# Performance work log

Measured on AMD Instinct MI355X. Metric: run time of the kernel, lower is better.

## Reference

```python
import jax, jax.numpy as jnp
import numpy as np
from jax import lax

B, H, W = 8, 500, 500
M = 2048          # per-image cap on active bottleneck voxels (ragged -> fixed)
GRID = 125        # bottleneck grid size
ENC_RANGE = 125.0
HEADS, ATTN_CH, CH = 4, 128, 64
EPS = 1e-5
NEG = -1e9

def _conv(x, w, b, stride, pad):
    y = lax.conv_general_dilated(x, w, (stride, stride), pad,
                                 dimension_numbers=('NCHW', 'HWIO', 'NCHW'))
    return y + b[None, :, None, None]

def _maxpool2(m):
    return lax.reduce_window(m, -jnp.inf, lax.max, (1, 1, 2, 2), (1, 1, 2, 2), 'VALID')

def setup_inputs():
    key = jax.random.key(0)
    ks = jax.random.split(key, 12)
    occ = (jax.random.uniform(ks[0], (B, 1, H, W)) < 0.005).astype(jnp.float32)
    x = jax.random.normal(ks[1], (B, 1, H, W), dtype=jnp.float32) * occ
    def rn(k, shape, scale):
        return jax.random.normal(k, shape, dtype=jnp.float32) * scale
    return {
        'x': x,
        'w0': rn(ks[2], (3, 3, 1, 32), 0.3), 'b0': jnp.zeros(32, jnp.float32),
        'g0': jnp.ones(32, jnp.float32), 'be0': jnp.zeros(32, jnp.float32),
        'w1': rn(ks[3], (2, 2, 32, 64), 0.1), 'b1': jnp.zeros(64, jnp.float32),
        'g1': jnp.ones(64, jnp.float32), 'be1': jnp.zeros(64, jnp.float32),
        'w2': rn(ks[4], (2, 2, 64, 64), 0.08), 'b2': jnp.zeros(64, jnp.float32),
        'g2': jnp.ones(64, jnp.float32), 'be2': jnp.zeros(64, jnp.float32),
        'wpe': rn(ks[5], (2, 2, CH), 0.5), 'bpe': jnp.zeros((2, CH), jnp.float32),
        'wq': rn(ks[6], (2, CH, ATTN_CH), 0.12), 'bq': jnp.zeros((2, ATTN_CH), jnp.float32),
        'wk': rn(ks[7], (2, CH, ATTN_CH), 0.12), 'bk': jnp.zeros((2, ATTN_CH), jnp.float32),
        'wv': rn(ks[8], (2, CH, ATTN_CH), 0.12), 'bv': jnp.zeros((2, ATTN_CH), jnp.float32),
        'wo': rn(ks[9], (2, ATTN_CH, CH), 0.09), 'bo': jnp.zeros((2, CH), jnp.float32),
        'wh': rn(ks[10], (CH, 4), 0.12), 'bh': jnp.zeros(4, jnp.float32),
    }

def reference(x, w0, b0, g0, be0, w1, b1, g1, be1, w2, b2, g2, be2,
              wpe, bpe, wq, bq, wk, bk, wv, bv, wo, bo, wh, bh):
    # active-site mask (Voxels.from_dense)
    mask0 = (x != 0).any(axis=1, keepdims=True).astype(x.dtype)   # [B,1,500,500]

    def bn_relu(y, g, be):
        # eval-mode BatchNorm1d over active voxel features (running stats 0/1)
        return jax.nn.relu(g[None, :, None, None] * y / jnp.sqrt(1.0 + EPS)
                           + be[None, :, None, None])

    # enc0: submanifold 3x3/s1 -> active set unchanged; inactive inputs are zero
    y = bn_relu(_conv(x, w0, b0, 1, 'SAME'), g0, be0) * mask0
    # enc1/enc2: strided 2x2/s2 -> output active iff any input in window active
    mask1 = _maxpool2(mask0)
    y = bn_relu(_conv(y, w1, b1, 2, 'VALID'), g1, be1) * mask1
    mask2 = _maxpool2(mask1)
    y = bn_relu(_conv(y, w2, b2, 2, 'VALID'), g2, be2) * mask2    # [B,64,125,125]

    # gather active bottleneck voxels per image (ragged -> fixed M + validity mask)
    mflat = mask2.reshape(B, GRID * GRID)
    vals, idx = lax.top_k(mflat, M)     # active-first; stable tie-break (lowest idx)
    valid = vals                        # [B,M] in {0,1}
    feats = jnp.take_along_axis(
        y.reshape(B, CH, GRID * GRID).transpose(0, 2, 1),
        idx[:, :, None], axis=1)        # [B,M,64]
    pos = jnp.stack([idx // GRID, idx % GRID], axis=-1).astype(x.dtype) / ENC_RANGE

    dh = ATTN_CH // HEADS
    kmask = (1.0 - valid)[:, None, None, :] * NEG
    for i in range(2):  # N_ATTN structurally distinct layers
        pe = pos @ wpe[i] + bpe[i]
        h = feats + pe
        q = (h @ wq[i] + bq[i]).reshape(B, M, HEADS, dh)
        k = (h @ wk[i] + bk[i]).reshape(B, M, HEADS, dh)
        v = (h @ wv[i] + bv[i]).reshape(B, M, HEADS, dh)
        s = jnp.einsum('bqhd,bkhd->bhqk', q, k) / jnp.sqrt(jnp.asarray(dh, x.dtype))
        a = jax.nn.softmax(s + kmask, axis=-1)
        o = jnp.einsum('bhqk,bkhd->bqhd', a, v).reshape(B, M, ATTN_CH)
        feats = (feats + o @ wo[i] + bo[i]) * valid[..., None]

    # sparse_global_avg_pool: mean over active voxels per image
    counts = jnp.clip(valid.sum(axis=1, keepdims=True), 1.0, None)
    pooled = feats.sum(axis=1) / counts                            # [B,64]
    return pooled @ wh + bh                                        # [B,4]
```

## Files before the change

kernel.cpp:

```cpp
#include <hip/hip_runtime.h>

#define BDIM   8
#define NPIX   250000
#define G1N    62500
#define G2N    15625
#define NB0    977
#define NB1    245
#define NB2    62
#define CAP0   4096
#define CAP1   4096
#define CAPM   2048
#define CH     64
#define ACH    128
#define NHEADS 4
#define DH     32

static constexpr float BN_INV    = 0.99999500003749969f;
static constexpr float ATT_SCALE = 0.17677669529663687f;

typedef _Float16 f16x8 __attribute__((ext_vector_type(8)));
typedef float f32x4 __attribute__((ext_vector_type(4)));

static constexpr size_t E_MAP0  = 0;
static constexpr size_t E_MAP1  = E_MAP0 + (size_t)BDIM*NPIX;
static constexpr size_t E_CNT   = E_MAP1 + (size_t)BDIM*G1N;
static constexpr size_t E_ZEND  = E_CNT + 32;
static constexpr size_t E_BC    = E_ZEND;
static constexpr size_t E_BO    = E_BC + (size_t)3*BDIM*1024;
static constexpr size_t E_BM    = E_BO + (size_t)3*BDIM*1024;
static constexpr size_t E_LIST0 = E_BM + (size_t)3*BDIM*1024*8;
static constexpr size_t E_LIST1 = E_LIST0 + (size_t)BDIM*CAP0;
static constexpr size_t E_LIST2 = E_LIST1 + (size_t)BDIM*CAP1;
static constexpr size_t E_Y0    = E_LIST2 + (size_t)BDIM*CAPM;
static constexpr size_t E_Y1    = E_Y0 + (size_t)BDIM*CAP0*32;
static constexpr size_t E_FE    = E_Y1 + (size_t)BDIM*CAP1*64;
static constexpr size_t E_QF    = E_FE + (size_t)BDIM*CAPM*64;
static constexpr size_t E_KF    = E_QF + (size_t)32*CAPM*32/2;
static constexpr size_t E_VT    = E_KF + (size_t)32*CAPM*32/2;
static constexpr size_t E_PART  = E_VT + (size_t)32*CAPM*32/2;


__device__ __forceinline__ bool act0(const float* x, int pix, int b) {
  return (pix < NPIX) && (x[(size_t)b * NPIX + pix] != 0.f);
}
__device__ __forceinline__ bool act1(const int* map0, int p, int b) {
  if (p >= G1N) return false;
  int i = p / 250, j = p - i * 250;
  const int* m = map0 + (size_t)b * NPIX + (2 * i) * 500 + 2 * j;
  return (m[0] | m[1] | m[500] | m[501]) != 0;
}
__device__ __forceinline__ bool act2(const int* map1, int p, int b) {
  if (p >= G2N) return false;
  int i = p / 125, j = p - i * 125;
  const int* m = map1 + (size_t)b * G1N + (2 * i) * 250 + 2 * j;
  return (m[0] | m[1] | m[250] | m[251]) != 0;
}

#define COUNT_BODY(ACT_EXPR)                                            \
  int idx = blockIdx.x * 256 + threadIdx.x;                             \
  int b = blockIdx.y;                                                   \
  bool act = (ACT_EXPR);                                                \
  unsigned long long mask = __ballot(act);                              \
  __shared__ int wc[4];                                                 \
  if ((threadIdx.x & 63) == 0) {                                        \
    wc[threadIdx.x >> 6] = __popcll(mask);                              \
    bm[((size_t)b * 1024 + blockIdx.x) * 4 + (threadIdx.x >> 6)] = mask;\
  }                                                                     \
  __syncthreads();                                                      \
  if (threadIdx.x == 0)                                                 \
    bcnt[b * 1024 + blockIdx.x] = wc[0] + wc[1] + wc[2] + wc[3];

__global__ void k_cnt0(const float* __restrict__ x, int* __restrict__ bcnt,
                       unsigned long long* __restrict__ bm) {
  COUNT_BODY(act0(x, idx, b))
}
__global__ void k_cnt1(const int* __restrict__ map0, int* __restrict__ bcnt,
                       unsigned long long* __restrict__ bm) {
  COUNT_BODY(act1(map0, idx, b))
}
__global__ void k_cnt2(const int* __restrict__ map1, int* __restrict__ bcnt,
                       unsigned long long* __restrict__ bm) {
  COUNT_BODY(act2(map1, idx, b))
}

__global__ __launch_bounds__(256) void k_scan(const int* __restrict__ bcnt,
                                              int* __restrict__ boff,
                                              int* __restrict__ cnt,
                                              int nblk, int cbase) {
  int b = blockIdx.x;
  int t = threadIdx.x;
  int base = t * 4;
  int v[4];
  int ts = 0;
#pragma unroll
  for (int u = 0; u < 4; ++u) {
    v[u] = (base + u < nblk) ? bcnt[b * 1024 + base + u] : 0;
    ts += v[u];
  }
  int lane = t & 63, w = t >> 6;
  int incl = ts;
#pragma unroll
  for (int off = 1; off < 64; off <<= 1) {
    int o = __shfl_up(incl, off, 64);
    if (lane >= off) incl += o;
  }
  __shared__ int wsum[4];
  if (lane == 63) wsum[w] = incl;
  __syncthreads();
  int woff = 0;
#pragma unroll
  for (int k = 0; k < 3; ++k) if (k < w) woff += wsum[k];
  int run = woff + incl - ts;
#pragma unroll
  for (int u = 0; u < 4; ++u) {
    if (base + u < nblk) boff[b * 1024 + base + u] = run;
    run += v[u];
  }
  if (t == 255) cnt[cbase + b] = run;
}

#define EMIT_PROLOG                                                     \
  int idx = blockIdx.x * 256 + threadIdx.x;                             \
  int b = blockIdx.y;                                                   \
  int lane = threadIdx.x & 63;                                          \
  unsigned long long mask =                                             \
      bm[((size_t)b * 1024 + blockIdx.x) * 4 + (threadIdx.x >> 6)];     \
  bool act = (mask >> lane) & 1;                                        \
  __shared__ int wbase[4];                                              \
  if (lane == 0) wbase[threadIdx.x >> 6] = __popcll(mask);              \
  __syncthreads();                                                      \
  if (threadIdx.x == 0) {                                               \
    int s = boff[b * 1024 + blockIdx.x];                                \
    for (int w = 0; w < 4; ++w) { int c = wbase[w]; wbase[w] = s; s += c; } \
  }                                                                     \
  __syncthreads();                                                      \
  int slot = wbase[threadIdx.x >> 6] + __popcll(mask & ((1ull << lane) - 1ull));

__global__ void k_emit0(const unsigned long long* __restrict__ bm,
                        const int* __restrict__ boff,
                        int* __restrict__ map0, int* __restrict__ list0) {
  EMIT_PROLOG
  if (act && slot < CAP0) {
    list0[b * CAP0 + slot] = idx;
    map0[(size_t)b * NPIX + idx] = slot + 1;
  }
}
__global__ void k_emit1(const unsigned long long* __restrict__ bm,
                        const int* __restrict__ boff,
                        int* __restrict__ map1, int* __restrict__ list1) {
  EMIT_PROLOG
  if (act && slot < CAP1) {
    list1[b * CAP1 + slot] = idx;
    map1[(size_t)b * G1N + idx] = slot + 1;
  }
}
__global__ void k_emit2(const unsigned long long* __restrict__ bm,
                        const int* __restrict__ boff,
                        int* __restrict__ list2) {
  EMIT_PROLOG
  if (act && slot < CAPM) list2[b * CAPM + slot] = idx;
}


__global__ void k_y0(const float* __restrict__ x, const float* __restrict__ w0,
                     const float* __restrict__ b0, const float* __restrict__ g0,
                     const float* __restrict__ be0,
                     const int* __restrict__ list0, const int* __restrict__ cnt,
                     float* __restrict__ y0) {
  int t = blockIdx.x * 256 + threadIdx.x;
  int b = t >> 17;
  int r = t & 131071;
  int slot = r >> 5, c = r & 31;
  int n = min(cnt[b], CAP0);
  if (slot >= n) return;
  int pix = list0[b * CAP0 + slot];
  int i = pix / 500, j = pix - i * 500;
  float acc = b0[c];
#pragma unroll
  for (int di = 0; di < 3; ++di) {
    int ii = i + di - 1;
    if ((unsigned)ii >= 500u) continue;
#pragma unroll
    for (int dj = 0; dj < 3; ++dj) {
      int jj = j + dj - 1;
      if ((unsigned)jj >= 500u) continue;
      acc += x[(size_t)b * NPIX + ii * 500 + jj] * w0[(di * 3 + dj) * 32 + c];
    }
  }
  float o = g0[c] * acc * BN_INV + be0[c];
  y0[((size_t)(b * CAP0) + slot) * 32 + c] = fmaxf(o, 0.f);
}

__global__ void k_y1(const float* __restrict__ y0, const float* __restrict__ w1,
                     const float* __restrict__ b1, const float* __restrict__ g1,
                     const float* __restrict__ be1,
                     const int* __restrict__ map0, const int* __restrict__ list1,
                     const int* __restrict__ cnt, float* __restrict__ y1) {
  int b = blockIdx.x >> 9;
  int sblk = blockIdx.x & 511;
  int s0 = sblk * 8;
  int n = min(cnt[BDIM + b], CAP1);
  if (s0 >= n) return;
  __shared__ float inT[4][32][8];
  for (int idx = threadIdx.x; idx < 1024; idx += 64) {
    int s = idx & 7;
    int r = idx >> 3;
    int ci = r & 31, pp = r >> 5;
    float v = 0.f;
    int sg = s0 + s;
    if (sg < n) {
      int p = list1[b * CAP1 + sg];
      int i = p / 250, j = p - i * 250;
      int sm = map0[(size_t)b * NPIX + (2 * i + (pp >> 1)) * 500 + (2 * j + (pp & 1))];
      if (sm) v = y0[((size_t)(b * CAP0) + (sm - 1)) * 32 + ci];
    }
    inT[pp][ci][s] = v;
  }
  __syncthreads();
  int co = threadIdx.x;
  float acc[8];
#pragma unroll
  for (int s = 0; s < 8; ++s) acc[s] = b1[co];
#pragma unroll 2
  for (int pp = 0; pp < 4; ++pp)
    for (int ci = 0; ci < 32; ++ci) {
      float wv = w1[((pp << 5) + ci) * 64 + co];
      float4 i0 = *(const float4*)&inT[pp][ci][0];
      float4 i1 = *(const float4*)&inT[pp][ci][4];
      acc[0] += i0.x * wv; acc[1] += i0.y * wv; acc[2] += i0.z * wv; acc[3] += i0.w * wv;
      acc[4] += i1.x * wv; acc[5] += i1.y * wv; acc[6] += i1.z * wv; acc[7] += i1.w * wv;
    }
  int smax = min(8, n - s0);
  for (int s = 0; s < smax; ++s) {
    float o = g1[co] * acc[s] * BN_INV + be1[co];
    y1[((size_t)(b * CAP1) + s0 + s) * 64 + co] = fmaxf(o, 0.f);
  }
}

__global__ void k_y2(const float* __restrict__ y1, const float* __restrict__ w2,
                     const float* __restrict__ b2, const float* __restrict__ g2,
                     const float* __restrict__ be2,
                     const int* __restrict__ map1, const int* __restrict__ list2,
                     const int* __restrict__ cnt, float* __restrict__ feats) {
  int b = blockIdx.x >> 8;
  int sblk = blockIdx.x & 255;
  int s0 = sblk * 8;
  int n = min(cnt[2 * BDIM + b], CAPM);
  if (s0 >= n) return;
  __shared__ float inT[4][64][8];
  for (int idx = threadIdx.x; idx < 2048; idx += 64) {
    int s = idx & 7;
    int r = idx >> 3;
    int ci = r & 63, pp = r >> 6;
    float v = 0.f;
    int sg = s0 + s;
    if (sg < n) {
      int p = list2[b * CAPM + sg];
      int i = p / 125, j = p - i * 125;
      int sm = map1[(size_t)b * G1N + (2 * i + (pp >> 1)) * 250 + (2 * j + (pp & 1))];
      if (sm) v = y1[((size_t)(b * CAP1) + (sm - 1)) * 64 + ci];
    }
    inT[pp][ci][s] = v;
  }
  __syncthreads();
  int co = threadIdx.x;
  float acc[8];
#pragma unroll
  for (int s = 0; s < 8; ++s) acc[s] = b2[co];
#pragma unroll 2
  for (int pp = 0; pp < 4; ++pp)
    for (int ci = 0; ci < 64; ++ci) {
      float wv = w2[((pp << 6) + ci) * 64 + co];
      float4 i0 = *(const float4*)&inT[pp][ci][0];
      float4 i1 = *(const float4*)&inT[pp][ci][4];
      acc[0] += i0.x * wv; acc[1] += i0.y * wv; acc[2] += i0.z * wv; acc[3] += i0.w * wv;
      acc[4] += i1.x * wv; acc[5] += i1.y * wv; acc[6] += i1.z * wv; acc[7] += i1.w * wv;
    }
  int smax = min(8, n - s0);
  for (int s = 0; s < smax; ++s) {
    float o = g2[co] * acc[s] * BN_INV + be2[co];
    feats[((size_t)(b * CAPM) + s0 + s) * 64 + co] = fmaxf(o, 0.f);
  }
}


__global__ void k_qkv(const float* __restrict__ feats, const int* __restrict__ list2,
                      const int* __restrict__ cnt,
                      const float* __restrict__ wpe, const float* __restrict__ bpe,
                      const float* __restrict__ wq, const float* __restrict__ bq,
                      const float* __restrict__ wk, const float* __restrict__ bk,
                      const float* __restrict__ wv, const float* __restrict__ bv,
                      int layer, _Float16* __restrict__ qf, _Float16* __restrict__ kf,
                      _Float16* __restrict__ vt) {
  int b = blockIdx.x >> 7;
  int sblk = blockIdx.x & 127;
  int s0 = sblk * 16;
  int n = min(cnt[2 * BDIM + b], CAPM);
  if (s0 >= n) return;
  __shared__ float hT[64][16];
  for (int idx = threadIdx.x; idx < 1024; idx += 128) {
    int s = idx & 15, c = idx >> 4;
    float hv = 0.f;
    int sg = s0 + s;
    if (sg < n) {
      int p = list2[b * CAPM + sg];
      int i = p / 125, j = p - i * 125;
      hv = feats[((size_t)(b * CAPM) + sg) * 64 + c]
         + (float)i * (1.f / 125.f) * wpe[(layer * 2 + 0) * 64 + c]
         + (float)j * (1.f / 125.f) * wpe[(layer * 2 + 1) * 64 + c]
         + bpe[layer * 64 + c];
    }
    hT[c][s] = hv;
  }
  __syncthreads();
  int o = threadIdx.x;
  float accq[16], acck[16], accv[16];
  float bqv = bq[layer * 128 + o], bkv = bk[layer * 128 + o], bvv = bv[layer * 128 + o];
#pragma unroll
  for (int s = 0; s < 16; ++s) { accq[s] = bqv; acck[s] = bkv; accv[s] = bvv; }
  const float* wq_ = wq + (size_t)layer * 64 * 128 + o;
  const float* wk_ = wk + (size_t)layer * 64 * 128 + o;
  const float* wv_ = wv + (size_t)layer * 64 * 128 + o;
  for (int c = 0; c < 64; ++c) {
    float wqv = wq_[c * 128], wkv = wk_[c * 128], wvv = wv_[c * 128];
    float hh[16];
#pragma unroll
    for (int sq = 0; sq < 4; ++sq) {
      float4 h4 = *(const float4*)&hT[c][4 * sq];
      hh[4 * sq] = h4.x; hh[4 * sq + 1] = h4.y; hh[4 * sq + 2] = h4.z; hh[4 * sq + 3] = h4.w;
    }
#pragma unroll
    for (int s = 0; s < 16; ++s) {
      accq[s] += hh[s] * wqv; acck[s] += hh[s] * wkv; accv[s] += hh[s] * wvv;
    }
  }
  int hd = o >> 5, d = o & 31;
  size_t bh = (size_t)(b * NHEADS + hd);
  int smax = min(16, n - s0);
  for (int s = 0; s < smax; ++s) {
    size_t rb = (bh * CAPM + s0 + s) * 32 + d;
    qf[rb] = (_Float16)accq[s];
    kf[rb] = (_Float16)acck[s];
    vt[(bh * 32 + d) * CAPM + s0 + s] = (_Float16)accv[s];
  }
}


union U4H8 { uint4 u; f16x8 h; };
union PKU  { _Float16 h[2]; unsigned int u; };

__global__ __launch_bounds__(256) void k_attn(
    const _Float16* __restrict__ qf, const _Float16* __restrict__ kf,
    const _Float16* __restrict__ vt, const int* __restrict__ cnt,
    const float* __restrict__ wo, const float* __restrict__ bo, int layer,
    float* __restrict__ feats) {
  int qt = blockIdx.x & 127;
  int b  = blockIdx.x >> 7;
  int n = min(cnt[2 * BDIM + b], CAPM);
  int q0 = qt * 16;
  if (q0 >= n) return;
  int h = threadIdx.x >> 6;
  int lane = threadIdx.x & 63;
  int g = lane >> 4, qr = lane & 15;
  size_t bh = (size_t)(b * NHEADS + h) * CAPM;
  const _Float16* vbase = vt + (size_t)(b * NHEADS + h) * 32 * CAPM;
  f16x8 fq = *(const f16x8*)(qf + (bh + q0 + qr) * 32 + g * 8);
  f32x4 acc0 = {0.f, 0.f, 0.f, 0.f}, acc1 = {0.f, 0.f, 0.f, 0.f};
  float m = -1e30f, l = 0.f;
  __shared__ unsigned int P4[4][512];
  __shared__ float Lf4[4][16];
  __shared__ float Ll4[4][16];
  __shared__ float oT[128][17];
  unsigned int* P = P4[h];
  float* Lf = Lf4[h];
  int swz = (qr & 7) << 2;

  for (int t0 = 0; t0 < n; t0 += 64) {
    f32x4 st[4];
#pragma unroll
    for (int t = 0; t < 4; ++t) {
      f16x8 ka = *(const f16x8*)(kf + (bh + t0 + 16 * t + qr) * 32 + g * 8);
      f32x4 z = {0.f, 0.f, 0.f, 0.f};
      st[t] = __builtin_amdgcn_mfma_f32_16x16x32_f16(ka, fq, z, 0, 0, 0);
    }
    if (t0 + 64 > n) {
#pragma unroll
      for (int t = 0; t < 4; ++t)
#pragma unroll
        for (int r = 0; r < 4; ++r)
          if (t0 + 16 * t + 4 * g + r >= n) st[t][r] = -1e30f;
    }
    float tm = -1e30f;
#pragma unroll
    for (int t = 0; t < 4; ++t)
#pragma unroll
      for (int r = 0; r < 4; ++r) tm = fmaxf(tm, st[t][r]);
    tm = fmaxf(tm, __shfl_xor(tm, 16));
    tm = fmaxf(tm, __shfl_xor(tm, 32));
    float mn = fmaxf(m, tm * ATT_SCALE);
    float f = __expf(m - mn);
    m = mn;
    if (g == 0) Lf[qr] = f;
    float ls = 0.f;
#pragma unroll
    for (int t = 0; t < 4; ++t) {
      PKU a, c;
      float p0 = __expf(st[t][0] * ATT_SCALE - mn);
      float p1 = __expf(st[t][1] * ATT_SCALE - mn);
      float p2 = __expf(st[t][2] * ATT_SCALE - mn);
      float p3 = __expf(st[t][3] * ATT_SCALE - mn);
      a.h[0] = (_Float16)p0; a.h[1] = (_Float16)p1;
      c.h[0] = (_Float16)p2; c.h[1] = (_Float16)p3;
      ls += (float)a.h[0] + (float)a.h[1] + (float)c.h[0] + (float)c.h[1];
      int w = qr * 32 + 8 * t + 2 * g;
      P[w ^ swz] = a.u;
      P[(w + 1) ^ swz] = c.u;
    }
    ls += __shfl_xor(ls, 16);
    ls += __shfl_xor(ls, 32);
    l = l * f + ls;
    __syncthreads();
    U4H8 pa0, pa1;
    pa0.u = *(const uint4*)&P[(qr * 32 + 4 * g) ^ swz];
    pa1.u = *(const uint4*)&P[(qr * 32 + 16 + 4 * g) ^ swz];
    float fr0 = Lf[4 * g + 0], fr1 = Lf[4 * g + 1];
    float fr2 = Lf[4 * g + 2], fr3 = Lf[4 * g + 3];
    acc0[0] *= fr0; acc0[1] *= fr1; acc0[2] *= fr2; acc0[3] *= fr3;
    acc1[0] *= fr0; acc1[1] *= fr1; acc1[2] *= fr2; acc1[3] *= fr3;
    __syncthreads();
    f16x8 v00 = *(const f16x8*)(vbase + (size_t)qr * CAPM + t0 + g * 8);
    f16x8 v01 = *(const f16x8*)(vbase + (size_t)(16 + qr) * CAPM + t0 + g * 8);
    f16x8 v10 = *(const f16x8*)(vbase + (size_t)qr * CAPM + t0 + 32 + g * 8);
    f16x8 v11 = *(const f16x8*)(vbase + (size_t)(16 + qr) * CAPM + t0 + 32 + g * 8);
    acc0 = __builtin_amdgcn_mfma_f32_16x16x32_f16(pa0.h, v00, acc0, 0, 0, 0);
    acc1 = __builtin_amdgcn_mfma_f32_16x16x32_f16(pa0.h, v01, acc1, 0, 0, 0);
    acc0 = __builtin_amdgcn_mfma_f32_16x16x32_f16(pa1.h, v10, acc0, 0, 0, 0);
    acc1 = __builtin_amdgcn_mfma_f32_16x16x32_f16(pa1.h, v11, acc1, 0, 0, 0);
  }
  if (g == 0) Ll4[h][qr] = l;
  __syncthreads();
#pragma unroll
  for (int r = 0; r < 4; ++r) {
    float inv = 1.f / Ll4[h][4 * g + r];
    oT[h * 32 + qr][4 * g + r] = acc0[r] * inv;
    oT[h * 32 + 16 + qr][4 * g + r] = acc1[r] * inv;
  }
  __syncthreads();
  int co = lane;
  float pacc[4] = {0.f, 0.f, 0.f, 0.f};
  const float* w = wo + (size_t)layer * 128 * 64 + co;
  for (int c = 0; c < 128; ++c) {
    float wv = w[c * 64];
#pragma unroll
    for (int u = 0; u < 4; ++u) pacc[u] += oT[c][4 * h + u] * wv;
  }
  float bov = bo[layer * 64 + co];
#pragma unroll
  for (int u = 0; u < 4; ++u) {
    int tok = q0 + 4 * h + u;
    if (tok < n) feats[((size_t)(b * CAPM) + tok) * 64 + co] += pacc[u] + bov;
  }
}


__global__ void k_head1(const float* __restrict__ feats, const int* __restrict__ cnt,
                        float* __restrict__ part) {
  int b = blockIdx.x >> 4;
  int chunk = blockIdx.x & 15;
  int n = min(cnt[2 * BDIM + b], CAPM);
  int c = threadIdx.x & 63, sub = threadIdx.x >> 6;
  int lo = chunk * 128, hi = min(n, lo + 128);
  float s = 0.f;
  for (int mm = lo + sub; mm < hi; mm += 4)
    s += feats[((size_t)(b * CAPM) + mm) * 64 + c];
  __shared__ float red[4][64];
  red[sub][c] = s;
  __syncthreads();
  if (threadIdx.x < 64)
    part[(b * 16 + chunk) * 64 + c] = red[0][c] + red[1][c] + red[2][c] + red[3][c];
}

__global__ void k_head2(const float* __restrict__ part, const float* __restrict__ wh,
                        const float* __restrict__ bhd, const int* __restrict__ cnt,
                        float* __restrict__ out) {
  int b = blockIdx.x;
  int n = min(cnt[2 * BDIM + b], CAPM);
  int c = threadIdx.x;
  float s = 0.f;
#pragma unroll
  for (int k = 0; k < 16; ++k) s += part[(b * 16 + k) * 64 + c];
  __shared__ float pooled[64];
  pooled[c] = s / (float)max(n, 1);
  __syncthreads();
  if (c < 4) {
    float o = bhd[c];
#pragma unroll
    for (int c2 = 0; c2 < 64; ++c2) o += pooled[c2] * wh[c2 * 4 + c];
    out[b * 4 + c] = o;
  }
}


extern "C" void kernel_launch(void* const* d_in, const int* in_sizes, int n_in,
                              void* d_out, int out_size, void* d_ws, size_t ws_size,
                              hipStream_t stream) {
  const float* x   = (const float*)d_in[0];
  const float* w0  = (const float*)d_in[1];
  const float* b0  = (const float*)d_in[2];
  const float* g0  = (const float*)d_in[3];
  const float* be0 = (const float*)d_in[4];
  const float* w1  = (const float*)d_in[5];
  const float* b1  = (const float*)d_in[6];
  const float* g1  = (const float*)d_in[7];
  const float* be1 = (const float*)d_in[8];
  const float* w2  = (const float*)d_in[9];
  const float* b2  = (const float*)d_in[10];
  const float* g2  = (const float*)d_in[11];
  const float* be2 = (const float*)d_in[12];
  const float* wpe = (const float*)d_in[13];
  const float* bpe = (const float*)d_in[14];
  const float* wq  = (const float*)d_in[15];
  const float* bq  = (const float*)d_in[16];
  const float* wk  = (const float*)d_in[17];
  const float* bk  = (const float*)d_in[18];
  const float* wv  = (const float*)d_in[19];
  const float* bv  = (const float*)d_in[20];
  const float* wo  = (const float*)d_in[21];
  const float* bo  = (const float*)d_in[22];
  const float* wh  = (const float*)d_in[23];
  const float* bh  = (const float*)d_in[24];

  int* wsI = (int*)d_ws;
  float* wsF = (float*)d_ws;
  unsigned long long* bm = (unsigned long long*)(wsI + E_BM);
  _Float16* qf = (_Float16*)(wsI + E_QF);
  _Float16* kf = (_Float16*)(wsI + E_KF);
  _Float16* vt = (_Float16*)(wsI + E_VT);

  hipMemsetAsync(d_ws, 0, E_ZEND * 4, stream);

  k_cnt0<<<dim3(NB0, BDIM), 256, 0, stream>>>(x, wsI + E_BC + 0 * BDIM * 1024,
                                              bm + 0 * BDIM * 4096);
  k_scan<<<BDIM, 256, 0, stream>>>(wsI + E_BC + 0 * BDIM * 1024,
                                   wsI + E_BO + 0 * BDIM * 1024,
                                   wsI + E_CNT, NB0, 0);
  k_emit0<<<dim3(NB0, BDIM), 256, 0, stream>>>(bm + 0 * BDIM * 4096,
                                               wsI + E_BO + 0 * BDIM * 1024,
                                               wsI + E_MAP0, wsI + E_LIST0);
  k_y0<<<(BDIM * CAP0 * 32) / 256, 256, 0, stream>>>(
      x, w0, b0, g0, be0, wsI + E_LIST0, wsI + E_CNT, wsF + E_Y0);
  k_cnt1<<<dim3(NB1, BDIM), 256, 0, stream>>>(wsI + E_MAP0,
                                              wsI + E_BC + 1 * BDIM * 1024,
                                              bm + 1 * BDIM * 4096);
  k_scan<<<BDIM, 256, 0, stream>>>(wsI + E_BC + 1 * BDIM * 1024,
                                   wsI + E_BO + 1 * BDIM * 1024,
                                   wsI + E_CNT, NB1, BDIM);
  k_emit1<<<dim3(NB1, BDIM), 256, 0, stream>>>(bm + 1 * BDIM * 4096,
                                               wsI + E_BO + 1 * BDIM * 1024,
                                               wsI + E_MAP1, wsI + E_LIST1);
  k_y1<<<BDIM * (CAP1 / 8), 64, 0, stream>>>(
      wsF + E_Y0, w1, b1, g1, be1, wsI + E_MAP0, wsI + E_LIST1, wsI + E_CNT, wsF + E_Y1);
  k_cnt2<<<dim3(NB2, BDIM), 256, 0, stream>>>(wsI + E_MAP1,
                                              wsI + E_BC + 2 * BDIM * 1024,
                                              bm + 2 * BDIM * 4096);
  k_scan<<<BDIM, 256, 0, stream>>>(wsI + E_BC + 2 * BDIM * 1024,
                                   wsI + E_BO + 2 * BDIM * 1024,
                                   wsI + E_CNT, NB2, 2 * BDIM);
  k_emit2<<<dim3(NB2, BDIM), 256, 0, stream>>>(bm + 2 * BDIM * 4096,
                                               wsI + E_BO + 2 * BDIM * 1024,
                                               wsI + E_LIST2);
  k_y2<<<BDIM * (CAPM / 8), 64, 0, stream>>>(
      wsF + E_Y1, w2, b2, g2, be2, wsI + E_MAP1, wsI + E_LIST2, wsI + E_CNT, wsF + E_FE);

  for (int layer = 0; layer < 2; ++layer) {
    k_qkv<<<BDIM * (CAPM / 16), 128, 0, stream>>>(
        wsF + E_FE, wsI + E_LIST2, wsI + E_CNT, wpe, bpe, wq, bq, wk, bk, wv, bv,
        layer, qf, kf, vt);
    k_attn<<<BDIM * (CAPM / 16), 256, 0, stream>>>(
        qf, kf, vt, wsI + E_CNT, wo, bo, layer, wsF + E_FE);
  }

  k_head1<<<BDIM * 16, 256, 0, stream>>>(wsF + E_FE, wsI + E_CNT, wsF + E_PART);
  k_head2<<<BDIM, 64, 0, stream>>>(wsF + E_PART, wh, bh, wsI + E_CNT, (float*)d_out);
}
```

Baseline: 292.8 us.

## Split attention into per-head wave blocks with prefetched K/V and separate projection

Attention now runs one 64-thread block per (batch, head, query tile) with no __syncthreads, double-buffers K and V register loads one tile ahead, and passes rescale factors with shuffles instead of shared memory. The output projection moves to a new k_proj kernel that reads an intermediate fp32 buffer. Block indices interleave the batch so images with different active counts spread across CUs. This aims at more parallelism and hidden memory latency, at the cost of an extra launch and a global round-trip of the attention output.

```diff
diff --git a/kernel.cpp b/kernel.cpp
--- a/kernel.cpp
+++ b/kernel.cpp
@@ -37,7 +37,8 @@
 static constexpr size_t E_QF    = E_FE + (size_t)BDIM*CAPM*64;
 static constexpr size_t E_KF    = E_QF + (size_t)32*CAPM*32/2;
 static constexpr size_t E_VT    = E_KF + (size_t)32*CAPM*32/2;
-static constexpr size_t E_PART  = E_VT + (size_t)32*CAPM*32/2;
+static constexpr size_t E_O     = E_VT + (size_t)32*CAPM*32/2;
+static constexpr size_t E_PART  = E_O + (size_t)BDIM*CAPM*ACH;
 
 
 __device__ __forceinline__ bool act0(const float* x, int pix, int b) {
@@ -292,8 +293,8 @@
                       const float* __restrict__ wv, const float* __restrict__ bv,
                       int layer, _Float16* __restrict__ qf, _Float16* __restrict__ kf,
                       _Float16* __restrict__ vt) {
-  int b = blockIdx.x >> 7;
-  int sblk = blockIdx.x & 127;
+  int b = blockIdx.x & 7;
+  int sblk = blockIdx.x >> 3;
   int s0 = sblk * 16;
   int n = min(cnt[2 * BDIM + b], CAPM);
   if (s0 >= n) return;
@@ -349,117 +350,183 @@
 union U4H8 { uint4 u; f16x8 h; };
 union PKU  { _Float16 h[2]; unsigned int u; };
 
-__global__ __launch_bounds__(256) void k_attn(
+#define LOADK(K0, K1, K2, K3, T0)                                          \
+  K0 = *(const f16x8*)(kf + (bh + (T0) + qr) * 32 + g8);                   \
+  K1 = *(const f16x8*)(kf + (bh + (T0) + 16 + qr) * 32 + g8);              \
+  K2 = *(const f16x8*)(kf + (bh + (T0) + 32 + qr) * 32 + g8);              \
+  K3 = *(const f16x8*)(kf + (bh + (T0) + 48 + qr) * 32 + g8);
+
+#define LOADV(V0, V1, V2, V3, T0)                                          \
+  V0 = *(const f16x8*)(vbase + (size_t)qr * CAPM + (T0) + g8);             \
+  V1 = *(const f16x8*)(vbase + (size_t)(16 + qr) * CAPM + (T0) + g8);      \
+  V2 = *(const f16x8*)(vbase + (size_t)qr * CAPM + (T0) + 32 + g8);        \
+  V3 = *(const f16x8*)(vbase + (size_t)(16 + qr) * CAPM + (T0) + 32 + g8);
+
+#define PROCESS(K0, K1, K2, K3, V0, V1, V2, V3, T0)                        \
+  {                                                                        \
+    f32x4 z = {0.f, 0.f, 0.f, 0.f};                                        \
+    f32x4 st0 = __builtin_amdgcn_mfma_f32_16x16x32_f16(K0, fq, z, 0, 0, 0);\
+    f32x4 st1 = __builtin_amdgcn_mfma_f32_16x16x32_f16(K1, fq, z, 0, 0, 0);\
+    f32x4 st2 = __builtin_amdgcn_mfma_f32_16x16x32_f16(K2, fq, z, 0, 0, 0);\
+    f32x4 st3 = __builtin_amdgcn_mfma_f32_16x16x32_f16(K3, fq, z, 0, 0, 0);\
+    if ((T0) + 64 > n) {                                                   \
+      _Pragma("unroll") for (int r = 0; r < 4; ++r) {                      \
+        if ((T0) + 4 * g + r >= n)      st0[r] = -1e30f;                   \
+        if ((T0) + 16 + 4 * g + r >= n) st1[r] = -1e30f;                   \
+        if ((T0) + 32 + 4 * g + r >= n) st2[r] = -1e30f;                   \
+        if ((T0) + 48 + 4 * g + r >= n) st3[r] = -1e30f;                   \
+      }                                                                    \
+    }                                                                      \
+    float tm = st0[0];                                                     \
+    _Pragma("unroll") for (int r = 1; r < 4; ++r) tm = fmaxf(tm, st0[r]);  \
+    _Pragma("unroll") for (int r = 0; r < 4; ++r) tm = fmaxf(tm, st1[r]);  \
+    _Pragma("unroll") for (int r = 0; r < 4; ++r) tm = fmaxf(tm, st2[r]);  \
+    _Pragma("unroll") for (int r = 0; r < 4; ++r) tm = fmaxf(tm, st3[r]);  \
+    tm = fmaxf(tm, __shfl_xor(tm, 16));                                    \
+    tm = fmaxf(tm, __shfl_xor(tm, 32));                                    \
+    float mn = fmaxf(m, tm * ATT_SCALE);                                   \
+    float f_ = __expf(m - mn);                                             \
+    m = mn;                                                                \
+    float ls = 0.f;                                                        \
+    {                                                                      \
+      PKU a, c;                                                            \
+      a.h[0] = (_Float16)__expf(st0[0] * ATT_SCALE - mn);                  \
+      a.h[1] = (_Float16)__expf(st0[1] * ATT_SCALE - mn);                  \
+      c.h[0] = (_Float16)__expf(st0[2] * ATT_SCALE - mn);                  \
+      c.h[1] = (_Float16)__expf(st0[3] * ATT_SCALE - mn);                  \
+      ls += (float)a.h[0] + (float)a.h[1] + (float)c.h[0] + (float)c.h[1]; \
+      P[(qr * 32 + 0 + 2 * g) ^ swz] = a.u;                                \
+      P[(qr * 32 + 1 + 2 * g) ^ swz] = c.u;                                \
+      a.h[0] = (_Float16)__expf(st1[0] * ATT_SCALE - mn);                  \
+      a.h[1] = (_Float16)__expf(st1[1] * ATT_SCALE - mn);                  \
+      c.h[0] = (_Float16)__expf(st1[2] * ATT_SCALE - mn);                  \
+      c.h[1] = (_Float16)__expf(st1[3] * ATT_SCALE - mn);                  \
+      ls += (float)a.h[0] + (float)a.h[1] + (float)c.h[0] + (float)c.h[1]; \
+      P[(qr * 32 + 8 + 2 * g) ^ swz] = a.u;                                \
+      P[(qr * 32 + 9 + 2 * g) ^ swz] = c.u;                                \
+      a.h[0] = (_Float16)__expf(st2[0] * ATT_SCALE - mn);                  \
+      a.h[1] = (_Float16)__expf(st2[1] * ATT_SCALE - mn);                  \
+      c.h[0] = (_Float16)__expf(st2[2] * ATT_SCALE - mn);                  \
+      c.h[1] = (_Float16)__expf(st2[3] * ATT_SCALE - mn);                  \
+      ls += (float)a.h[0] + (float)a.h[1] + (float)c.h[0] + (float)c.h[1]; \
+      P[(qr * 32 + 16 + 2 * g) ^ swz] = a.u;                               \
+      P[(qr * 32 + 17 + 2 * g) ^ swz] = c.u;                               \
+      a.h[0] = (_Float16)__expf(st3[0] * ATT_SCALE - mn);                  \
+      a.h[1] = (_Float16)__expf(st3[1] * ATT_SCALE - mn);                  \
+      c.h[0] = (_Float16)__expf(st3[2] * ATT_SCALE - mn);                  \
+      c.h[1] = (_Float16)__expf(st3[3] * ATT_SCALE - mn);                  \
+      ls += (float)a.h[0] + (float)a.h[1] + (float)c.h[0] + (float)c.h[1]; \
+      P[(qr * 32 + 24 + 2 * g) ^ swz] = a.u;                               \
+      P[(qr * 32 + 25 + 2 * g) ^ swz] = c.u;                               \
+    }                                                                      \
+    ls += __shfl_xor(ls, 16);                                              \
+    ls += __shfl_xor(ls, 32);                                              \
+    l = l * f_ + ls;                                                       \
+    __builtin_amdgcn_sched_barrier(0);                                     \
+    U4H8 pa0, pa1;                                                         \
+    pa0.u = *(const uint4*)&P[(qr * 32 + 4 * g) ^ swz];                    \
+    pa1.u = *(const uint4*)&P[(qr * 32 + 16 + 4 * g) ^ swz];               \
+    float fr0 = __shfl(f_, 4 * g + 0, 16);                                 \
+    float fr1 = __shfl(f_, 4 * g + 1, 16);                                 \
+    float fr2 = __shfl(f_, 4 * g + 2, 16);                                 \
+    float fr3 = __shfl(f_, 4 * g + 3, 16);                                 \
+    acc0[0] *= fr0; acc0[1] *= fr1; acc0[2] *= fr2; acc0[3] *= fr3;        \
+    acc1[0] *= fr0; acc1[1] *= fr1; acc1[2] *= fr2; acc1[3] *= fr3;        \
+    acc0 = __builtin_amdgcn_mfma_f32_16x16x32_f16(pa0.h, V0, acc0, 0, 0, 0);\
+    acc1 = __builtin_amdgcn_mfma_f32_16x16x32_f16(pa0.h, V1, acc1, 0, 0, 0);\
+    acc0 = __builtin_amdgcn_mfma_f32_16x16x32_f16(pa1.h, V2, acc0, 0, 0, 0);\
+    acc1 = __builtin_amdgcn_mfma_f32_16x16x32_f16(pa1.h, V3, acc1, 0, 0, 0);\
+  }
+
+__global__ __launch_bounds__(64, 4) void k_attn(
     const _Float16* __restrict__ qf, const _Float16* __restrict__ kf,
     const _Float16* __restrict__ vt, const int* __restrict__ cnt,
-    const float* __restrict__ wo, const float* __restrict__ bo, int layer,
-    float* __restrict__ feats) {
-  int qt = blockIdx.x & 127;
-  int b  = blockIdx.x >> 7;
+    float* __restrict__ obuf) {
+  int b  = blockIdx.x & 7;
+  int rr = blockIdx.x >> 3;
+  int qt = rr & 127;
+  int h  = rr >> 7;
   int n = min(cnt[2 * BDIM + b], CAPM);
   int q0 = qt * 16;
   if (q0 >= n) return;
-  int h = threadIdx.x >> 6;
-  int lane = threadIdx.x & 63;
+  int lane = threadIdx.x;
   int g = lane >> 4, qr = lane & 15;
+  int g8 = g * 8;
   size_t bh = (size_t)(b * NHEADS + h) * CAPM;
   const _Float16* vbase = vt + (size_t)(b * NHEADS + h) * 32 * CAPM;
-  f16x8 fq = *(const f16x8*)(qf + (bh + q0 + qr) * 32 + g * 8);
+  f16x8 fq = *(const f16x8*)(qf + (bh + q0 + qr) * 32 + g8);
   f32x4 acc0 = {0.f, 0.f, 0.f, 0.f}, acc1 = {0.f, 0.f, 0.f, 0.f};
   float m = -1e30f, l = 0.f;
-  __shared__ unsigned int P4[4][512];
-  __shared__ float Lf4[4][16];
-  __shared__ float Ll4[4][16];
-  __shared__ float oT[128][17];
-  unsigned int* P = P4[h];
-  float* Lf = Lf4[h];
+  __shared__ unsigned int P[512];
   int swz = (qr & 7) << 2;
 
-  for (int t0 = 0; t0 < n; t0 += 64) {
-    f32x4 st[4];
-#pragma unroll
-    for (int t = 0; t < 4; ++t) {
-      f16x8 ka = *(const f16x8*)(kf + (bh + t0 + 16 * t + qr) * 32 + g * 8);
-      f32x4 z = {0.f, 0.f, 0.f, 0.f};
-      st[t] = __builtin_amdgcn_mfma_f32_16x16x32_f16(ka, fq, z, 0, 0, 0);
-    }
-    if (t0 + 64 > n) {
-#pragma unroll
-      for (int t = 0; t < 4; ++t)
-#pragma unroll
-        for (int r = 0; r < 4; ++r)
-          if (t0 + 16 * t + 4 * g + r >= n) st[t][r] = -1e30f;
-    }
-    float tm = -1e30f;
-#pragma unroll
-    for (int t = 0; t < 4; ++t)
-#pragma unroll
-      for (int r = 0; r < 4; ++r) tm = fmaxf(tm, st[t][r]);
-    tm = fmaxf(tm, __shfl_xor(tm, 16));
-    tm = fmaxf(tm, __shfl_xor(tm, 32));
-    float mn = fmaxf(m, tm * ATT_SCALE);
-    float f = __expf(m - mn);
-    m = mn;
-    if (g == 0) Lf[qr] = f;
-    float ls = 0.f;
-#pragma unroll
-    for (int t = 0; t < 4; ++t) {
-      PKU a, c;
-      float p0 = __expf(st[t][0] * ATT_SCALE - mn);
-      float p1 = __expf(st[t][1] * ATT_SCALE - mn);
-      float p2 = __expf(st[t][2] * ATT_SCALE - mn);
-      float p3 = __expf(st[t][3] * ATT_SCALE - mn);
-      a.h[0] = (_Float16)p0; a.h[1] = (_Float16)p1;
-      c.h[0] = (_Float16)p2; c.h[1] = (_Float16)p3;
-      ls += (float)a.h[0] + (float)a.h[1] + (float)c.h[0] + (float)c.h[1];
-      int w = qr * 32 + 8 * t + 2 * g;
-      P[w ^ swz] = a.u;
-      P[(w + 1) ^ swz] = c.u;
-    }
-    ls += __shfl_xor(ls, 16);
-    ls += __shfl_xor(ls, 32);
-    l = l * f + ls;
-    __syncthreads();
-    U4H8 pa0, pa1;
-    pa0.u = *(const uint4*)&P[(qr * 32 + 4 * g) ^ swz];
-    pa1.u = *(const uint4*)&P[(qr * 32 + 16 + 4 * g) ^ swz];
-    float fr0 = Lf[4 * g + 0], fr1 = Lf[4 * g + 1];
-    float fr2 = Lf[4 * g + 2], fr3 = Lf[4 * g + 3];
-    acc0[0] *= fr0; acc0[1] *= fr1; acc0[2] *= fr2; acc0[3] *= fr3;
-    acc1[0] *= fr0; acc1[1] *= fr1; acc1[2] *= fr2; acc1[3] *= fr3;
-    __syncthreads();
-    f16x8 v00 = *(const f16x8*)(vbase + (size_t)qr * CAPM + t0 + g * 8);
-    f16x8 v01 = *(const f16x8*)(vbase + (size_t)(16 + qr) * CAPM + t0 + g * 8);
-    f16x8 v10 = *(const f16x8*)(vbase + (size_t)qr * CAPM + t0 + 32 + g * 8);
-    f16x8 v11 = *(const f16x8*)(vbase + (size_t)(16 + qr) * CAPM + t0 + 32 + g * 8);
-    acc0 = __builtin_amdgcn_mfma_f32_16x16x32_f16(pa0.h, v00, acc0, 0, 0, 0);
-    acc1 = __builtin_amdgcn_mfma_f32_16x16x32_f16(pa0.h, v01, acc1, 0, 0, 0);
-    acc0 = __builtin_amdgcn_mfma_f32_16x16x32_f16(pa1.h, v10, acc0, 0, 0, 0);
-    acc1 = __builtin_amdgcn_mfma_f32_16x16x32_f16(pa1.h, v11, acc1, 0, 0, 0);
-  }
-  if (g == 0) Ll4[h][qr] = l;
+  int nt = (n + 63) >> 6;
+  f16x8 ka0, ka1, ka2, ka3, va0, va1, va2, va3;
+  f16x8 kb0, kb1, kb2, kb3, vb0, vb1, vb2, vb3;
+  LOADK(ka0, ka1, ka2, ka3, 0)
+  LOADV(va0, va1, va2, va3, 0)
+  for (int t = 0; t < nt; t += 2) {
+    if (t + 1 < nt) {
+      LOADK(kb0, kb1, kb2, kb3, (t + 1) * 64)
+      LOADV(vb0, vb1, vb2, vb3, (t + 1) * 64)
+    }
+    PROCESS(ka0, ka1, ka2, ka3, va0, va1, va2, va3, t * 64)
+    if (t + 1 < nt) {
+      if (t + 2 < nt) {
+        LOADK(ka0, ka1, ka2, ka3, (t + 2) * 64)
+        LOADV(va0, va1, va2, va3, (t + 2) * 64)
+      }
+      PROCESS(kb0, kb1, kb2, kb3, vb0, vb1, vb2, vb3, (t + 1) * 64)
+    }
+  }
+#pragma unroll
+  for (int r = 0; r < 4; ++r) {
+    float inv = 1.f / __shfl(l, 4 * g + r, 16);
+    int tok = q0 + 4 * g + r;
+    if (tok < n) {
+      float* op = obuf + ((size_t)b * CAPM + tok) * ACH + h * DH;
+      op[qr] = acc0[r] * inv;
+      op[16 + qr] = acc1[r] * inv;
+    }
+  }
+}
+
+
+__global__ void k_proj(const float* __restrict__ obuf, const float* __restrict__ wo,
+                       const float* __restrict__ bo, const int* __restrict__ cnt,
+                       int layer, float* __restrict__ feats) {
+  int b = blockIdx.x & 7;
+  int sblk = blockIdx.x >> 3;
+  int s0 = sblk * 16;
+  int n = min(cnt[2 * BDIM + b], CAPM);
+  if (s0 >= n) return;
+  __shared__ float oT[128][16];
+  for (int idx = threadIdx.x; idx < 2048; idx += 64) {
+    int s = idx & 15, c = idx >> 4;
+    int sg = s0 + s;
+    oT[c][s] = (sg < n) ? obuf[((size_t)b * CAPM + sg) * ACH + c] : 0.f;
+  }
   __syncthreads();
-#pragma unroll
-  for (int r = 0; r < 4; ++r) {
-    float inv = 1.f / Ll4[h][4 * g + r];
-    oT[h * 32 + qr][4 * g + r] = acc0[r] * inv;
-    oT[h * 32 + 16 + qr][4 * g + r] = acc1[r] * inv;
-  }
-  __syncthreads();
-  int co = lane;
-  float pacc[4] = {0.f, 0.f, 0.f, 0.f};
+  int co = threadIdx.x;
+  float acc[16];
+#pragma unroll
+  for (int s = 0; s < 16; ++s) acc[s] = 0.f;
   const float* w = wo + (size_t)layer * 128 * 64 + co;
   for (int c = 0; c < 128; ++c) {
     float wv = w[c * 64];
-#pragma unroll
-    for (int u = 0; u < 4; ++u) pacc[u] += oT[c][4 * h + u] * wv;
+    float hh[16];
+#pragma unroll
+    for (int sq = 0; sq < 4; ++sq) {
+      float4 h4 = *(const float4*)&oT[c][4 * sq];
+      hh[4 * sq] = h4.x; hh[4 * sq + 1] = h4.y; hh[4 * sq + 2] = h4.z; hh[4 * sq + 3] = h4.w;
+    }
+#pragma unroll
+    for (int s = 0; s < 16; ++s) acc[s] += hh[s] * wv;
   }
   float bov = bo[layer * 64 + co];
-#pragma unroll
-  for (int u = 0; u < 4; ++u) {
-    int tok = q0 + 4 * h + u;
-    if (tok < n) feats[((size_t)(b * CAPM) + tok) * 64 + co] += pacc[u] + bov;
-  }
+  int smax = min(16, n - s0);
+  for (int s = 0; s < smax; ++s)
+    feats[((size_t)(b * CAPM) + s0 + s) * 64 + co] += acc[s] + bov;
 }
 
 
@@ -576,8 +643,10 @@
     k_qkv<<<BDIM * (CAPM / 16), 128, 0, stream>>>(
         wsF + E_FE, wsI + E_LIST2, wsI + E_CNT, wpe, bpe, wq, bq, wk, bk, wv, bv,
         layer, qf, kf, vt);
-    k_attn<<<BDIM * (CAPM / 16), 256, 0, stream>>>(
-        qf, kf, vt, wsI + E_CNT, wo, bo, layer, wsF + E_FE);
+    k_attn<<<BDIM * NHEADS * (CAPM / 16), 64, 0, stream>>>(
+        qf, kf, vt, wsI + E_CNT, wsF + E_O);
+    k_proj<<<BDIM * (CAPM / 16), 64, 0, stream>>>(
+        wsF + E_O, wo, bo, wsI + E_CNT, layer, wsF + E_FE);
   }
 
   k_head1<<<BDIM * 16, 256, 0, stream>>>(wsF + E_FE, wsI + E_CNT, wsF + E_PART);
```

Result: slower. 301.1 us (+2.8%).
